# Kernel tuning notes

Hardware: AMD Instinct MI355X
Metric: run time of the kernel (lower is better)

Reference implementation:

```python
import jax, jax.numpy as jnp
import numpy as np

N_NODES = 100000
N_EDGES = 1600000
F_IN, F_HID, F_OUT = 48, 16, 16
K = 2  # kernel_size, dim=1, degree=1 open B-spline -> basis (1-u, u)


def glorot(key, shape):
    fan_in, fan_out = shape[-2], shape[-1]
    s = jnp.sqrt(6.0 / (fan_in + fan_out))
    return jax.random.uniform(key, shape, jnp.float32, -s, s)


def setup_inputs() -> dict:
    key = jax.random.key(0)
    ks = jax.random.split(key, 10)
    x = jax.random.normal(ks[0], (N_NODES, F_IN), jnp.float32)
    edge_attr = jax.random.uniform(ks[1], (N_EDGES, 1), jnp.float32)
    edge_index = jax.random.randint(ks[2], (2, N_EDGES), 0, N_NODES, jnp.int64)
    W1 = glorot(ks[3], (K, F_IN, F_HID))
    root1 = glorot(ks[4], (F_IN, F_HID))
    b1 = jnp.zeros((F_HID,), jnp.float32)
    W2 = glorot(ks[5], (K, F_HID, F_OUT))
    root2 = glorot(ks[6], (F_HID, F_OUT))
    b2 = jnp.zeros((F_OUT,), jnp.float32)
    return {"x": x, "edge_attr": edge_attr, "edge_index": edge_index,
            "W1": W1, "root1": root1, "b1": b1, "W2": W2, "root2": root2, "b2": b2}


def spline_conv(x, edge_index, u, W, root, bias, num_nodes):
    # x: [N,Fin], u: [E] pseudo coords in [0,1], W: [2,Fin,Fout]
    src, dst = edge_index[0], edge_index[1]
    xj = x[src]                                        # [E,Fin] gather
    m = jnp.einsum('ef,kfo->eko', xj, W)               # [E,2,Fout]
    basis = jnp.stack([1.0 - u, u], axis=1)            # linear open B-spline, K=2
    msg = jnp.einsum('ek,eko->eo', basis, m)           # [E,Fout]
    agg = jax.ops.segment_sum(msg, dst, num_segments=num_nodes)
    cnt = jax.ops.segment_sum(jnp.ones_like(msg[:, 0]), dst, num_segments=num_nodes)
    agg = agg / jnp.maximum(cnt, 1.0)[:, None]         # aggr='mean'
    return agg + x @ root + bias                       # root_weight + bias


def reference(x, edge_attr, edge_index, W1, root1, b1, W2, root2, b2):
    u = edge_attr[:, 0]
    h = jax.nn.elu(spline_conv(x, edge_index, u, W1, root1, b1, N_NODES))
    out = spline_conv(h, edge_index, u, W2, root2, b2, N_NODES)
    return jax.nn.log_softmax(out, axis=1)
```

## Files before the change

kernel.cpp:

```cpp
#include <hip/hip_runtime.h>
#include <math.h>

#define N_NODES 100000
#define N_EDGES 1600000
#define NBUK 782
#define BNODES 128
#define CAPSH 12
#define CAP 4096
#define NCHUNK 512
#define CPE 3125
#define NTBLK 1563
#define WS 52
#define RPW (BNODES + 1)

#define SM_LCUR   0
#define SM_GBASE  3128
#define SM_SC     6256
#define SM_UPK    10352
#define SM_SPK    22852
#define SM_UBUK   35352
#define SM_SBUK   41602
#define SM_UDL    47852
#define SM_SDL    50977
#define SM_TOTAL  54144

#define NTL(p) __builtin_nontemporal_load(p)

__device__ __forceinline__ unsigned bf16_rne(float x) {
    unsigned u = __float_as_uint(x);
    return (u + 0x7FFFu + ((u >> 16) & 1u)) >> 16;
}

__device__ __forceinline__ void accq(float acc[4], uint4 w, float uu) {
    acc[0] += fmaf(uu, __uint_as_float(w.x & 0xFFFF0000u), __uint_as_float(w.x << 16));
    acc[1] += fmaf(uu, __uint_as_float(w.y & 0xFFFF0000u), __uint_as_float(w.y << 16));
    acc[2] += fmaf(uu, __uint_as_float(w.z & 0xFFFF0000u), __uint_as_float(w.z << 16));
    acc[3] += fmaf(uu, __uint_as_float(w.w & 0xFFFF0000u), __uint_as_float(w.w << 16));
}

__global__ __launch_bounds__(1024)
void fused_transform_scatter(const float* __restrict__ X,
                             const float* __restrict__ W,
                             const float* __restrict__ root,
                             const float* __restrict__ bias,
                             unsigned* __restrict__ YPH, float* __restrict__ R,
                             const int* __restrict__ src,
                             const int* __restrict__ dst,
                             const float* __restrict__ u,
                             int* __restrict__ cursor,
                             unsigned* __restrict__ pkb,
                             unsigned char* __restrict__ dlb) {
    extern __shared__ char smem[];
    int t = threadIdx.x;
    if (blockIdx.x < NCHUNK) {
        int c = blockIdx.x;
        int* lcur            = (int*)(smem + SM_LCUR);
        int* gbase           = (int*)(smem + SM_GBASE);
        int* sc              = (int*)(smem + SM_SC);
        unsigned* upk        = (unsigned*)(smem + SM_UPK);
        unsigned* spk        = (unsigned*)(smem + SM_SPK);
        unsigned short* ubuk = (unsigned short*)(smem + SM_UBUK);
        unsigned short* sbuk = (unsigned short*)(smem + SM_SBUK);
        unsigned char* udl   = (unsigned char*)(smem + SM_UDL);
        unsigned char* sdl   = (unsigned char*)(smem + SM_SDL);

        for (int i = t; i < NBUK; i += 1024) lcur[i] = 0;
        __syncthreads();
        for (int j = t; j < CPE; j += 1024) {
            int e = c * CPE + j;
            int d = NTL(dst + e);
            float uu = NTL(u + e);
            uu = uu < 0.0f ? 0.0f : (uu > 1.0f ? 1.0f : uu);
            int u15 = (int)fmaf(uu, 32767.0f, 0.5f);
            upk[j] = (unsigned)NTL(src + e) | ((unsigned)u15 << 17);
            udl[j] = (unsigned char)(d & 127);
            int b = d >> 7;
            ubuk[j] = (unsigned short)b;
            atomicAdd(&lcur[b], 1);
        }
        __syncthreads();

        int v = (t < NBUK) ? lcur[t] : 0;
        sc[t] = v;
        __syncthreads();
        for (int off = 1; off < 1024; off <<= 1) {
            int x = (t >= off) ? sc[t - off] : 0;
            __syncthreads();
            sc[t] += x;
            __syncthreads();
        }
        if (t < NBUK) {
            int ex = sc[t] - v;
            lcur[t] = ex;
            int base = (t << CAPSH) + atomicAdd(&cursor[t], v);
            gbase[t] = base - ex;
        }
        __syncthreads();

        for (int j = t; j < CPE; j += 1024) {
            int b = ubuk[j];
            int p = atomicAdd(&lcur[b], 1);
            spk[p] = upk[j];
            sdl[p] = udl[j];
            sbuk[p] = (unsigned short)b;
        }
        __syncthreads();

        for (int j = t; j < CPE; j += 1024) {
            int b = sbuk[j];
            int g = gbase[b] + j;
            if (g < ((b + 1) << CAPSH)) {
                pkb[g] = spk[j];
                dlb[g] = sdl[j];
            }
        }
    } else {
        float* sW0 = (float*)smem;
        float* sWd = (float*)(smem + 3328);
        float* sR  = (float*)(smem + 6656);
        float* sB  = (float*)(smem + 9984);
        int bid = blockIdx.x - NCHUNK;
        for (int i = t; i < 48 * 16; i += 1024) {
            int f = i >> 4, o = i & 15;
            float w0 = W[i];
            float w1 = W[48 * 16 + i];
            sW0[o * WS + f] = w0;
            sWd[o * WS + f] = w1 - w0;
            sR[o * WS + f]  = root[i];
        }
        if (t < 16) sB[t] = bias[t];
        __syncthreads();

        int idx = bid * 1024 + t;
        int n = idx >> 4;
        int o = idx & 15;
        if (n >= N_NODES) return;

        const float4* xr  = (const float4*)(X + (long)n * 48);
        const float4* w0p = (const float4*)(sW0 + o * WS);
        const float4* wdp = (const float4*)(sWd + o * WS);
        const float4* wrp = (const float4*)(sR  + o * WS);
        float a0 = 0.0f, a1 = 0.0f, ar = 0.0f;
#pragma unroll
        for (int fc = 0; fc < 12; ++fc) {
            float4 xv = xr[fc];
            float4 w0 = w0p[fc];
            float4 wd = wdp[fc];
            float4 wr = wrp[fc];
            a0 = fmaf(xv.x, w0.x, a0); a0 = fmaf(xv.y, w0.y, a0);
            a0 = fmaf(xv.z, w0.z, a0); a0 = fmaf(xv.w, w0.w, a0);
            a1 = fmaf(xv.x, wd.x, a1); a1 = fmaf(xv.y, wd.y, a1);
            a1 = fmaf(xv.z, wd.z, a1); a1 = fmaf(xv.w, wd.w, a1);
            ar = fmaf(xv.x, wr.x, ar); ar = fmaf(xv.y, wr.y, ar);
            ar = fmaf(xv.z, wr.z, ar); ar = fmaf(xv.w, wr.w, ar);
        }
        YPH[idx] = bf16_rne(a0) | (bf16_rne(a1) << 16);
        R[idx]   = ar + sB[o];
    }
}

__global__ __launch_bounds__(512)
void aggregate1(const int* __restrict__ cursor,
                unsigned* __restrict__ pkb,
                const unsigned char* __restrict__ dlb,
                int* __restrict__ rptab,
                const uint4* __restrict__ YPH1,
                const float* __restrict__ R1,
                const float* __restrict__ W2,
                const float* __restrict__ root2,
                const float* __restrict__ b2,
                unsigned* __restrict__ YPH2,
                float* __restrict__ R2) {
    __shared__ unsigned spk[CAP];
    __shared__ int rp[RPW];
    __shared__ int cur[BNODES];
    __shared__ float sW0[256], sWd[256], sR[256], sB[16];
    int t = threadIdx.x, b = blockIdx.x;

    if (t < 256) {
        float w0 = W2[t], w1 = W2[256 + t];
        sW0[t] = w0;
        sWd[t] = w1 - w0;
        sR[t]  = root2[t];
    }
    if (t < 16) sB[t] = b2[t];
    if (t < BNODES) cur[t] = 0;
    __syncthreads();

    int cnt = cursor[b];
    if (cnt > CAP) cnt = CAP;
    unsigned* pk = pkb + ((size_t)b << CAPSH);
    const unsigned char* dl = dlb + ((size_t)b << CAPSH);
    int n4 = cnt >> 2, tail = cnt & 3, base4 = cnt & ~3;

    for (int j4 = t; j4 < n4; j4 += 512) {
        unsigned w = NTL((const unsigned*)dl + j4);
        atomicAdd(&cur[w & 255], 1);
        atomicAdd(&cur[(w >> 8) & 255], 1);
        atomicAdd(&cur[(w >> 16) & 255], 1);
        atomicAdd(&cur[w >> 24], 1);
    }
    if (t < tail) atomicAdd(&cur[NTL(dl + base4 + t)], 1);
    __syncthreads();

    int v = 0;
    if (t < BNODES) { v = cur[t]; rp[t] = v; }
    __syncthreads();
    for (int off = 1; off < BNODES; off <<= 1) {
        int x = 0;
        if (t < BNODES && t >= off) x = rp[t - off];
        __syncthreads();
        if (t < BNODES) rp[t] += x;
        __syncthreads();
    }
    if (t < BNODES) { int ex = rp[t] - v; rp[t] = ex; cur[t] = ex; }
    if (t == 0) rp[BNODES] = cnt;
    __syncthreads();

    for (int j4 = t; j4 < n4; j4 += 512) {
        uint4 p = ((const uint4*)pk)[j4];
        unsigned w = NTL((const unsigned*)dl + j4);
        spk[atomicAdd(&cur[w & 255], 1)]         = p.x;
        spk[atomicAdd(&cur[(w >> 8) & 255], 1)]  = p.y;
        spk[atomicAdd(&cur[(w >> 16) & 255], 1)] = p.z;
        spk[atomicAdd(&cur[w >> 24], 1)]         = p.w;
    }
    if (t < tail) {
        int j = base4 + t;
        spk[atomicAdd(&cur[NTL(dl + j)], 1)] = pk[j];
    }
    __syncthreads();

    for (int j = t; j < cnt; j += 512) pk[j] = spk[j];
    if (t < RPW) rptab[b * RPW + t] = rp[t];

    int node = t >> 2, q = t & 3;
    int n = (b << 7) + node;
    int beg = rp[node], end = rp[node + 1];
    int deg = end - beg;
    const float C = 1.0f / 32767.0f;

    float acc[4] = {0.0f, 0.0f, 0.0f, 0.0f};
    int j = beg;
    for (; j + 3 < end; j += 4) {
        unsigned p0 = spk[j], p1 = spk[j + 1], p2 = spk[j + 2], p3 = spk[j + 3];
        uint4 w0 = YPH1[(size_t)(p0 & 0x1FFFFu) * 4 + q];
        uint4 w1 = YPH1[(size_t)(p1 & 0x1FFFFu) * 4 + q];
        uint4 w2 = YPH1[(size_t)(p2 & 0x1FFFFu) * 4 + q];
        uint4 w3 = YPH1[(size_t)(p3 & 0x1FFFFu) * 4 + q];
        accq(acc, w0, (float)(p0 >> 17) * C);
        accq(acc, w1, (float)(p1 >> 17) * C);
        accq(acc, w2, (float)(p2 >> 17) * C);
        accq(acc, w3, (float)(p3 >> 17) * C);
    }
    for (; j < end; ++j) {
        unsigned p = spk[j];
        uint4 w = YPH1[(size_t)(p & 0x1FFFFu) * 4 + q];
        accq(acc, w, (float)(p >> 17) * C);
    }

    if (n < N_NODES) {
        float inv = 1.0f / (deg > 0 ? (float)deg : 1.0f);
        float4 rr = ((const float4*)(R1 + (size_t)n * 16))[q];
        float hq[4], w;
        w = fmaf(acc[0], inv, rr.x); hq[0] = w > 0.0f ? w : expm1f(w);
        w = fmaf(acc[1], inv, rr.y); hq[1] = w > 0.0f ? w : expm1f(w);
        w = fmaf(acc[2], inv, rr.z); hq[2] = w > 0.0f ? w : expm1f(w);
        w = fmaf(acc[3], inv, rr.w); hq[3] = w > 0.0f ? w : expm1f(w);

        int qbase = (t & 63) & ~3;
        float h16[16];
#pragma unroll
        for (int p = 0; p < 4; ++p) {
            h16[4 * p + 0] = __shfl(hq[0], qbase + p);
            h16[4 * p + 1] = __shfl(hq[1], qbase + p);
            h16[4 * p + 2] = __shfl(hq[2], qbase + p);
            h16[4 * p + 3] = __shfl(hq[3], qbase + p);
        }

        float a0[4] = {0, 0, 0, 0}, a1[4] = {0, 0, 0, 0}, ar[4] = {0, 0, 0, 0};
        int o0 = q * 4;
#pragma unroll
        for (int f = 0; f < 16; ++f) {
            float hv = h16[f];
#pragma unroll
            for (int o = 0; o < 4; ++o) {
                a0[o] = fmaf(hv, sW0[f * 16 + o0 + o], a0[o]);
                a1[o] = fmaf(hv, sWd[f * 16 + o0 + o], a1[o]);
                ar[o] = fmaf(hv, sR [f * 16 + o0 + o], ar[o]);
            }
        }
        uint4 yw;
        yw.x = bf16_rne(a0[0]) | (bf16_rne(a1[0]) << 16);
        yw.y = bf16_rne(a0[1]) | (bf16_rne(a1[1]) << 16);
        yw.z = bf16_rne(a0[2]) | (bf16_rne(a1[2]) << 16);
        yw.w = bf16_rne(a0[3]) | (bf16_rne(a1[3]) << 16);
        ((uint4*)YPH2)[(size_t)n * 4 + q] = yw;
        float4 rv;
        rv.x = ar[0] + sB[o0 + 0];
        rv.y = ar[1] + sB[o0 + 1];
        rv.z = ar[2] + sB[o0 + 2];
        rv.w = ar[3] + sB[o0 + 3];
        ((float4*)R2)[(size_t)n * 4 + q] = rv;
    }
}

__global__ __launch_bounds__(512)
void aggregate2(const int* __restrict__ rptab,
                const unsigned* __restrict__ pkb,
                const uint4* __restrict__ YPH2,
                const float* __restrict__ R2,
                float* __restrict__ out) {
    __shared__ int rp[RPW];
    int t = threadIdx.x, b = blockIdx.x;

    if (t < RPW) rp[t] = rptab[b * RPW + t];
    __syncthreads();

    const unsigned* pk = pkb + ((size_t)b << CAPSH);
    int node = t >> 2, q = t & 3;
    int n = (b << 7) + node;
    int beg = rp[node], end = rp[node + 1];
    int deg = end - beg;
    const float C = 1.0f / 32767.0f;

    float acc[4] = {0.0f, 0.0f, 0.0f, 0.0f};
    int j = beg;
    for (; j + 3 < end; j += 4) {
        unsigned p0 = pk[j], p1 = pk[j + 1], p2 = pk[j + 2], p3 = pk[j + 3];
        uint4 w0 = YPH2[(size_t)(p0 & 0x1FFFFu) * 4 + q];
        uint4 w1 = YPH2[(size_t)(p1 & 0x1FFFFu) * 4 + q];
        uint4 w2 = YPH2[(size_t)(p2 & 0x1FFFFu) * 4 + q];
        uint4 w3 = YPH2[(size_t)(p3 & 0x1FFFFu) * 4 + q];
        accq(acc, w0, (float)(p0 >> 17) * C);
        accq(acc, w1, (float)(p1 >> 17) * C);
        accq(acc, w2, (float)(p2 >> 17) * C);
        accq(acc, w3, (float)(p3 >> 17) * C);
    }
    for (; j < end; ++j) {
        unsigned p = pk[j];
        uint4 w = YPH2[(size_t)(p & 0x1FFFFu) * 4 + q];
        accq(acc, w, (float)(p >> 17) * C);
    }

    if (n < N_NODES) {
        float inv = 1.0f / (deg > 0 ? (float)deg : 1.0f);
        float4 rr = ((const float4*)R2)[(size_t)n * 4 + q];
        float v0 = fmaf(acc[0], inv, rr.x);
        float v1 = fmaf(acc[1], inv, rr.y);
        float v2 = fmaf(acc[2], inv, rr.z);
        float v3 = fmaf(acc[3], inv, rr.w);
        float m = fmaxf(fmaxf(v0, v1), fmaxf(v2, v3));
        m = fmaxf(m, __shfl_xor(m, 1));
        m = fmaxf(m, __shfl_xor(m, 2));
        float s = expf(v0 - m) + expf(v1 - m) + expf(v2 - m) + expf(v3 - m);
        s += __shfl_xor(s, 1);
        s += __shfl_xor(s, 2);
        float lse = m + logf(s);
        float4 ov = make_float4(v0 - lse, v1 - lse, v2 - lse, v3 - lse);
        ((float4*)out)[(size_t)n * 4 + q] = ov;
    }
}

extern "C" void kernel_launch(void* const* d_in, const int* in_sizes, int n_in,
                              void* d_out, int out_size, void* d_ws, size_t ws_size,
                              hipStream_t stream) {
    const float* x         = (const float*)d_in[0];
    const float* edge_attr = (const float*)d_in[1];
    const int*   edge_idx  = (const int*)d_in[2];
    const float* W1        = (const float*)d_in[3];
    const float* root1     = (const float*)d_in[4];
    const float* b1        = (const float*)d_in[5];
    const float* W2        = (const float*)d_in[6];
    const float* root2     = (const float*)d_in[7];
    const float* b2        = (const float*)d_in[8];
    float* out = (float*)d_out;

    const int* src = edge_idx;
    const int* dst = edge_idx + N_EDGES;

    char* ws = (char*)d_ws;
    unsigned*      pkb    = (unsigned*)(ws);
    unsigned char* dlb    = (unsigned char*)(ws + 12812288);
    unsigned*      YPH1   = (unsigned*)(ws + 16015360);
    float*         R1     = (float*)(ws + 22415360);
    unsigned*      YPH2   = (unsigned*)(ws + 28815360);
    float*         R2     = (float*)(ws + 35215360);
    int*           cursor = (int*)(ws + 41615360);
    int*           rptab  = (int*)(ws + 41618496);

    hipMemsetAsync(cursor, 0, NBUK * sizeof(int), stream);

    fused_transform_scatter<<<dim3(NCHUNK + NTBLK), 1024, SM_TOTAL, stream>>>(
        x, W1, root1, b1, YPH1, R1, src, dst, edge_attr, cursor, pkb, dlb);

    aggregate1<<<dim3(NBUK), 512, 0, stream>>>(
        cursor, pkb, dlb, rptab, (const uint4*)YPH1, R1, W2, root2, b2, YPH2, R2);

    aggregate2<<<dim3(NBUK), 512, 0, stream>>>(
        rptab, pkb, (const uint4*)YPH2, R2, out);
}
```

Baseline: 179.7 us.

## Replace LDS-staged edge bucketing with global atomics and split node aggregation across lane pairs

```diff
diff --git a/kernel.cpp b/kernel.cpp
--- a/kernel.cpp
+++ b/kernel.cpp
@@ -7,24 +7,16 @@
 #define BNODES 128
 #define CAPSH 12
 #define CAP 4096
-#define NCHUNK 512
-#define CPE 3125
+#define NSBLK 391
 #define NTBLK 1563
 #define WS 52
 #define RPW (BNODES + 1)
-
-#define SM_LCUR   0
-#define SM_GBASE  3128
-#define SM_SC     6256
-#define SM_UPK    10352
-#define SM_SPK    22852
-#define SM_UBUK   35352
-#define SM_SBUK   41602
-#define SM_UDL    47852
-#define SM_SDL    50977
-#define SM_TOTAL  54144
+#define SM_TRANSFORM 10048
 
 #define NTL(p) __builtin_nontemporal_load(p)
+
+typedef int   i32x4 __attribute__((ext_vector_type(4)));
+typedef float f32x4 __attribute__((ext_vector_type(4)));
 
 __device__ __forceinline__ unsigned bf16_rne(float x) {
     unsigned u = __float_as_uint(x);
@@ -52,66 +44,27 @@
                              unsigned char* __restrict__ dlb) {
     extern __shared__ char smem[];
     int t = threadIdx.x;
-    if (blockIdx.x < NCHUNK) {
-        int c = blockIdx.x;
-        int* lcur            = (int*)(smem + SM_LCUR);
-        int* gbase           = (int*)(smem + SM_GBASE);
-        int* sc              = (int*)(smem + SM_SC);
-        unsigned* upk        = (unsigned*)(smem + SM_UPK);
-        unsigned* spk        = (unsigned*)(smem + SM_SPK);
-        unsigned short* ubuk = (unsigned short*)(smem + SM_UBUK);
-        unsigned short* sbuk = (unsigned short*)(smem + SM_SBUK);
-        unsigned char* udl   = (unsigned char*)(smem + SM_UDL);
-        unsigned char* sdl   = (unsigned char*)(smem + SM_SDL);
-
-        for (int i = t; i < NBUK; i += 1024) lcur[i] = 0;
-        __syncthreads();
-        for (int j = t; j < CPE; j += 1024) {
-            int e = c * CPE + j;
-            int d = NTL(dst + e);
-            float uu = NTL(u + e);
-            uu = uu < 0.0f ? 0.0f : (uu > 1.0f ? 1.0f : uu);
-            int u15 = (int)fmaf(uu, 32767.0f, 0.5f);
-            upk[j] = (unsigned)NTL(src + e) | ((unsigned)u15 << 17);
-            udl[j] = (unsigned char)(d & 127);
-            int b = d >> 7;
-            ubuk[j] = (unsigned short)b;
-            atomicAdd(&lcur[b], 1);
-        }
-        __syncthreads();
-
-        int v = (t < NBUK) ? lcur[t] : 0;
-        sc[t] = v;
-        __syncthreads();
-        for (int off = 1; off < 1024; off <<= 1) {
-            int x = (t >= off) ? sc[t - off] : 0;
-            __syncthreads();
-            sc[t] += x;
-            __syncthreads();
-        }
-        if (t < NBUK) {
-            int ex = sc[t] - v;
-            lcur[t] = ex;
-            int base = (t << CAPSH) + atomicAdd(&cursor[t], v);
-            gbase[t] = base - ex;
-        }
-        __syncthreads();
-
-        for (int j = t; j < CPE; j += 1024) {
-            int b = ubuk[j];
-            int p = atomicAdd(&lcur[b], 1);
-            spk[p] = upk[j];
-            sdl[p] = udl[j];
-            sbuk[p] = (unsigned short)b;
-        }
-        __syncthreads();
-
-        for (int j = t; j < CPE; j += 1024) {
-            int b = sbuk[j];
-            int g = gbase[b] + j;
-            if (g < ((b + 1) << CAPSH)) {
-                pkb[g] = spk[j];
-                dlb[g] = sdl[j];
+    if (blockIdx.x < NSBLK) {
+        int gid = blockIdx.x * 1024 + t;
+        int e = gid * 4;
+        if (e < N_EDGES) {
+            i32x4 s4 = NTL((const i32x4*)src + gid);
+            i32x4 d4 = NTL((const i32x4*)dst + gid);
+            f32x4 u4 = NTL((const f32x4*)u + gid);
+#pragma unroll
+            for (int k = 0; k < 4; ++k) {
+                int d = d4[k];
+                float uu = u4[k];
+                uu = uu < 0.0f ? 0.0f : (uu > 1.0f ? 1.0f : uu);
+                int u15 = (int)fmaf(uu, 32767.0f, 0.5f);
+                unsigned pk = (unsigned)s4[k] | ((unsigned)u15 << 17);
+                int b = d >> 7;
+                int off = atomicAdd(&cursor[b], 1);
+                if (off < CAP) {
+                    int g = (b << CAPSH) + off;
+                    pkb[g] = pk;
+                    dlb[g] = (unsigned char)(d & 127);
+                }
             }
         }
     } else {
@@ -119,7 +72,7 @@
         float* sWd = (float*)(smem + 3328);
         float* sR  = (float*)(smem + 6656);
         float* sB  = (float*)(smem + 9984);
-        int bid = blockIdx.x - NCHUNK;
+        int bid = blockIdx.x - NSBLK;
         for (int i = t; i < 48 * 16; i += 1024) {
             int f = i >> 4, o = i & 15;
             float w0 = W[i];
@@ -159,7 +112,7 @@
     }
 }
 
-__global__ __launch_bounds__(512)
+__global__ __launch_bounds__(1024)
 void aggregate1(const int* __restrict__ cursor,
                 unsigned* __restrict__ pkb,
                 const unsigned char* __restrict__ dlb,
@@ -193,7 +146,7 @@
     const unsigned char* dl = dlb + ((size_t)b << CAPSH);
     int n4 = cnt >> 2, tail = cnt & 3, base4 = cnt & ~3;
 
-    for (int j4 = t; j4 < n4; j4 += 512) {
+    for (int j4 = t; j4 < n4; j4 += 1024) {
         unsigned w = NTL((const unsigned*)dl + j4);
         atomicAdd(&cur[w & 255], 1);
         atomicAdd(&cur[(w >> 8) & 255], 1);
@@ -217,7 +170,7 @@
     if (t == 0) rp[BNODES] = cnt;
     __syncthreads();
 
-    for (int j4 = t; j4 < n4; j4 += 512) {
+    for (int j4 = t; j4 < n4; j4 += 1024) {
         uint4 p = ((const uint4*)pk)[j4];
         unsigned w = NTL((const unsigned*)dl + j4);
         spk[atomicAdd(&cur[w & 255], 1)]         = p.x;
@@ -231,19 +184,19 @@
     }
     __syncthreads();
 
-    for (int j = t; j < cnt; j += 512) pk[j] = spk[j];
+    for (int j = t; j < cnt; j += 1024) pk[j] = spk[j];
     if (t < RPW) rptab[b * RPW + t] = rp[t];
 
-    int node = t >> 2, q = t & 3;
+    int node = t >> 3, lane3 = t & 7, q = lane3 & 3, h = lane3 >> 2;
     int n = (b << 7) + node;
     int beg = rp[node], end = rp[node + 1];
     int deg = end - beg;
     const float C = 1.0f / 32767.0f;
 
     float acc[4] = {0.0f, 0.0f, 0.0f, 0.0f};
-    int j = beg;
-    for (; j + 3 < end; j += 4) {
-        unsigned p0 = spk[j], p1 = spk[j + 1], p2 = spk[j + 2], p3 = spk[j + 3];
+    int j = beg + h;
+    for (; j + 6 < end; j += 8) {
+        unsigned p0 = spk[j], p1 = spk[j + 2], p2 = spk[j + 4], p3 = spk[j + 6];
         uint4 w0 = YPH1[(size_t)(p0 & 0x1FFFFu) * 4 + q];
         uint4 w1 = YPH1[(size_t)(p1 & 0x1FFFFu) * 4 + q];
         uint4 w2 = YPH1[(size_t)(p2 & 0x1FFFFu) * 4 + q];
@@ -253,11 +206,13 @@
         accq(acc, w2, (float)(p2 >> 17) * C);
         accq(acc, w3, (float)(p3 >> 17) * C);
     }
-    for (; j < end; ++j) {
+    for (; j < end; j += 2) {
         unsigned p = spk[j];
         uint4 w = YPH1[(size_t)(p & 0x1FFFFu) * 4 + q];
         accq(acc, w, (float)(p >> 17) * C);
     }
+#pragma unroll
+    for (int i = 0; i < 4; ++i) acc[i] += __shfl_xor(acc[i], 4);
 
     if (n < N_NODES) {
         float inv = 1.0f / (deg > 0 ? (float)deg : 1.0f);
@@ -268,14 +223,14 @@
         w = fmaf(acc[2], inv, rr.z); hq[2] = w > 0.0f ? w : expm1f(w);
         w = fmaf(acc[3], inv, rr.w); hq[3] = w > 0.0f ? w : expm1f(w);
 
-        int qbase = (t & 63) & ~3;
+        int b8 = (t & 63) & ~7;
         float h16[16];
 #pragma unroll
         for (int p = 0; p < 4; ++p) {
-            h16[4 * p + 0] = __shfl(hq[0], qbase + p);
-            h16[4 * p + 1] = __shfl(hq[1], qbase + p);
-            h16[4 * p + 2] = __shfl(hq[2], qbase + p);
-            h16[4 * p + 3] = __shfl(hq[3], qbase + p);
+            h16[4 * p + 0] = __shfl(hq[0], b8 + p);
+            h16[4 * p + 1] = __shfl(hq[1], b8 + p);
+            h16[4 * p + 2] = __shfl(hq[2], b8 + p);
+            h16[4 * p + 3] = __shfl(hq[3], b8 + p);
         }
 
         float a0[4] = {0, 0, 0, 0}, a1[4] = {0, 0, 0, 0}, ar[4] = {0, 0, 0, 0};
@@ -290,22 +245,24 @@
                 ar[o] = fmaf(hv, sR [f * 16 + o0 + o], ar[o]);
             }
         }
-        uint4 yw;
-        yw.x = bf16_rne(a0[0]) | (bf16_rne(a1[0]) << 16);
-        yw.y = bf16_rne(a0[1]) | (bf16_rne(a1[1]) << 16);
-        yw.z = bf16_rne(a0[2]) | (bf16_rne(a1[2]) << 16);
-        yw.w = bf16_rne(a0[3]) | (bf16_rne(a1[3]) << 16);
-        ((uint4*)YPH2)[(size_t)n * 4 + q] = yw;
-        float4 rv;
-        rv.x = ar[0] + sB[o0 + 0];
-        rv.y = ar[1] + sB[o0 + 1];
-        rv.z = ar[2] + sB[o0 + 2];
-        rv.w = ar[3] + sB[o0 + 3];
-        ((float4*)R2)[(size_t)n * 4 + q] = rv;
-    }
-}
-
-__global__ __launch_bounds__(512)
+        if (h == 0) {
+            uint4 yw;
+            yw.x = bf16_rne(a0[0]) | (bf16_rne(a1[0]) << 16);
+            yw.y = bf16_rne(a0[1]) | (bf16_rne(a1[1]) << 16);
+            yw.z = bf16_rne(a0[2]) | (bf16_rne(a1[2]) << 16);
+            yw.w = bf16_rne(a0[3]) | (bf16_rne(a1[3]) << 16);
+            ((uint4*)YPH2)[(size_t)n * 4 + q] = yw;
+            float4 rv;
+            rv.x = ar[0] + sB[o0 + 0];
+            rv.y = ar[1] + sB[o0 + 1];
+            rv.z = ar[2] + sB[o0 + 2];
+            rv.w = ar[3] + sB[o0 + 3];
+            ((float4*)R2)[(size_t)n * 4 + q] = rv;
+        }
+    }
+}
+
+__global__ __launch_bounds__(1024)
 void aggregate2(const int* __restrict__ rptab,
                 const unsigned* __restrict__ pkb,
                 const uint4* __restrict__ YPH2,
@@ -318,16 +275,17 @@
     __syncthreads();
 
     const unsigned* pk = pkb + ((size_t)b << CAPSH);
-    int node = t >> 2, q = t & 3;
+    int node = t >> 3, lane3 = t & 7, q = lane3 & 3, h = lane3 >> 2;
     int n = (b << 7) + node;
     int beg = rp[node], end = rp[node + 1];
     int deg = end - beg;
     const float C = 1.0f / 32767.0f;
 
     float acc[4] = {0.0f, 0.0f, 0.0f, 0.0f};
-    int j = beg;
-    for (; j + 3 < end; j += 4) {
-        unsigned p0 = pk[j], p1 = pk[j + 1], p2 = pk[j + 2], p3 = pk[j + 3];
+    int j = beg + h;
+    for (; j + 6 < end; j += 8) {
+        unsigned p0 = NTL(pk + j), p1 = NTL(pk + j + 2);
+        unsigned p2 = NTL(pk + j + 4), p3 = NTL(pk + j + 6);
         uint4 w0 = YPH2[(size_t)(p0 & 0x1FFFFu) * 4 + q];
         uint4 w1 = YPH2[(size_t)(p1 & 0x1FFFFu) * 4 + q];
         uint4 w2 = YPH2[(size_t)(p2 & 0x1FFFFu) * 4 + q];
@@ -337,11 +295,13 @@
         accq(acc, w2, (float)(p2 >> 17) * C);
         accq(acc, w3, (float)(p3 >> 17) * C);
     }
-    for (; j < end; ++j) {
-        unsigned p = pk[j];
+    for (; j < end; j += 2) {
+        unsigned p = NTL(pk + j);
         uint4 w = YPH2[(size_t)(p & 0x1FFFFu) * 4 + q];
         accq(acc, w, (float)(p >> 17) * C);
     }
+#pragma unroll
+    for (int i = 0; i < 4; ++i) acc[i] += __shfl_xor(acc[i], 4);
 
     if (n < N_NODES) {
         float inv = 1.0f / (deg > 0 ? (float)deg : 1.0f);
@@ -357,8 +317,10 @@
         s += __shfl_xor(s, 1);
         s += __shfl_xor(s, 2);
         float lse = m + logf(s);
-        float4 ov = make_float4(v0 - lse, v1 - lse, v2 - lse, v3 - lse);
-        ((float4*)out)[(size_t)n * 4 + q] = ov;
+        if (h == 0) {
+            float4 ov = make_float4(v0 - lse, v1 - lse, v2 - lse, v3 - lse);
+            ((float4*)out)[(size_t)n * 4 + q] = ov;
+        }
     }
 }
 
@@ -391,12 +353,12 @@
 
     hipMemsetAsync(cursor, 0, NBUK * sizeof(int), stream);
 
-    fused_transform_scatter<<<dim3(NCHUNK + NTBLK), 1024, SM_TOTAL, stream>>>(
+    fused_transform_scatter<<<dim3(NSBLK + NTBLK), 1024, SM_TRANSFORM, stream>>>(
         x, W1, root1, b1, YPH1, R1, src, dst, edge_attr, cursor, pkb, dlb);
 
-    aggregate1<<<dim3(NBUK), 512, 0, stream>>>(
+    aggregate1<<<dim3(NBUK), 1024, 0, stream>>>(
         cursor, pkb, dlb, rptab, (const uint4*)YPH1, R1, W2, root2, b2, YPH2, R2);
 
-    aggregate2<<<dim3(NBUK), 512, 0, stream>>>(
+    aggregate2<<<dim3(NBUK), 1024, 0, stream>>>(
         rptab, pkb, (const uint4*)YPH2, R2, out);
 }
```

Result: slower. 530.2 us (+195.0%).

## Pack edge payload and full dst into single 64-bit record with smaller bucket capacity

Applied to the files above, without the earlier changes.

```diff
diff --git a/kernel.cpp b/kernel.cpp
--- a/kernel.cpp
+++ b/kernel.cpp
@@ -5,24 +5,20 @@
 #define N_EDGES 1600000
 #define NBUK 782
 #define BNODES 128
-#define CAPSH 12
-#define CAP 4096
+#define CAP 2560
+#define CAPB (CAP * 8)
 #define NCHUNK 512
 #define CPE 3125
 #define NTBLK 1563
 #define WS 52
 #define RPW (BNODES + 1)
 
-#define SM_LCUR   0
-#define SM_GBASE  3128
-#define SM_SC     6256
-#define SM_UPK    10352
-#define SM_SPK    22852
-#define SM_UBUK   35352
-#define SM_SBUK   41602
-#define SM_UDL    47852
-#define SM_SDL    50977
-#define SM_TOTAL  54144
+#define SM_LCUR  0
+#define SM_GBASE 3128
+#define SM_SC    6256
+#define SM_UPDL  10352
+#define SM_SPDL  35352
+#define SM_TOTAL 60352
 
 #define NTL(p) __builtin_nontemporal_load(p)
 
@@ -48,21 +44,16 @@
                              const int* __restrict__ dst,
                              const float* __restrict__ u,
                              int* __restrict__ cursor,
-                             unsigned* __restrict__ pkb,
-                             unsigned char* __restrict__ dlb) {
+                             unsigned long long* __restrict__ pkd) {
     extern __shared__ char smem[];
     int t = threadIdx.x;
     if (blockIdx.x < NCHUNK) {
         int c = blockIdx.x;
-        int* lcur            = (int*)(smem + SM_LCUR);
-        int* gbase           = (int*)(smem + SM_GBASE);
-        int* sc              = (int*)(smem + SM_SC);
-        unsigned* upk        = (unsigned*)(smem + SM_UPK);
-        unsigned* spk        = (unsigned*)(smem + SM_SPK);
-        unsigned short* ubuk = (unsigned short*)(smem + SM_UBUK);
-        unsigned short* sbuk = (unsigned short*)(smem + SM_SBUK);
-        unsigned char* udl   = (unsigned char*)(smem + SM_UDL);
-        unsigned char* sdl   = (unsigned char*)(smem + SM_SDL);
+        int* lcur = (int*)(smem + SM_LCUR);
+        int* gbase = (int*)(smem + SM_GBASE);
+        int* sc = (int*)(smem + SM_SC);
+        unsigned long long* updl = (unsigned long long*)(smem + SM_UPDL);
+        unsigned long long* spdl = (unsigned long long*)(smem + SM_SPDL);
 
         for (int i = t; i < NBUK; i += 1024) lcur[i] = 0;
         __syncthreads();
@@ -72,11 +63,10 @@
             float uu = NTL(u + e);
             uu = uu < 0.0f ? 0.0f : (uu > 1.0f ? 1.0f : uu);
             int u15 = (int)fmaf(uu, 32767.0f, 0.5f);
-            upk[j] = (unsigned)NTL(src + e) | ((unsigned)u15 << 17);
-            udl[j] = (unsigned char)(d & 127);
-            int b = d >> 7;
-            ubuk[j] = (unsigned short)b;
-            atomicAdd(&lcur[b], 1);
+            unsigned pk32 = (unsigned)NTL(src + e) | ((unsigned)u15 << 17);
+            updl[j] = (unsigned long long)pk32 |
+                      ((unsigned long long)(unsigned)d << 32);
+            atomicAdd(&lcur[d >> 7], 1);
         }
         __syncthreads();
 
@@ -92,27 +82,25 @@
         if (t < NBUK) {
             int ex = sc[t] - v;
             lcur[t] = ex;
-            int base = (t << CAPSH) + atomicAdd(&cursor[t], v);
+            int base = t * CAP + atomicAdd(&cursor[t], v);
             gbase[t] = base - ex;
         }
         __syncthreads();
 
         for (int j = t; j < CPE; j += 1024) {
-            int b = ubuk[j];
+            unsigned long long w = updl[j];
+            int b = (int)(w >> 39) & 0x3FF;
             int p = atomicAdd(&lcur[b], 1);
-            spk[p] = upk[j];
-            sdl[p] = udl[j];
-            sbuk[p] = (unsigned short)b;
+            spdl[p] = w;
         }
         __syncthreads();
 
         for (int j = t; j < CPE; j += 1024) {
-            int b = sbuk[j];
+            unsigned long long w = spdl[j];
+            int b = (int)(w >> 39) & 0x3FF;
             int g = gbase[b] + j;
-            if (g < ((b + 1) << CAPSH)) {
-                pkb[g] = spk[j];
-                dlb[g] = sdl[j];
-            }
+            if (g < (b + 1) * CAP)
+                pkd[g] = w;
         }
     } else {
         float* sW0 = (float*)smem;
@@ -161,8 +149,7 @@
 
 __global__ __launch_bounds__(512)
 void aggregate1(const int* __restrict__ cursor,
-                unsigned* __restrict__ pkb,
-                const unsigned char* __restrict__ dlb,
+                unsigned long long* __restrict__ pkd,
                 int* __restrict__ rptab,
                 const uint4* __restrict__ YPH1,
                 const float* __restrict__ R1,
@@ -171,6 +158,7 @@
                 const float* __restrict__ b2,
                 unsigned* __restrict__ YPH2,
                 float* __restrict__ R2) {
+    __shared__ unsigned long long updl[CAP];
     __shared__ unsigned spk[CAP];
     __shared__ int rp[RPW];
     __shared__ int cur[BNODES];
@@ -189,18 +177,14 @@
 
     int cnt = cursor[b];
     if (cnt > CAP) cnt = CAP;
-    unsigned* pk = pkb + ((size_t)b << CAPSH);
-    const unsigned char* dl = dlb + ((size_t)b << CAPSH);
-    int n4 = cnt >> 2, tail = cnt & 3, base4 = cnt & ~3;
-
-    for (int j4 = t; j4 < n4; j4 += 512) {
-        unsigned w = NTL((const unsigned*)dl + j4);
-        atomicAdd(&cur[w & 255], 1);
-        atomicAdd(&cur[(w >> 8) & 255], 1);
-        atomicAdd(&cur[(w >> 16) & 255], 1);
-        atomicAdd(&cur[w >> 24], 1);
-    }
-    if (t < tail) atomicAdd(&cur[NTL(dl + base4 + t)], 1);
+    unsigned long long* gp =
+        (unsigned long long*)((char*)pkd + (size_t)b * CAPB);
+
+    for (int j = t; j < cnt; j += 512) {
+        unsigned long long w = NTL(gp + j);
+        updl[j] = w;
+        atomicAdd(&cur[(int)(w >> 32) & 127], 1);
+    }
     __syncthreads();
 
     int v = 0;
@@ -217,21 +201,15 @@
     if (t == 0) rp[BNODES] = cnt;
     __syncthreads();
 
-    for (int j4 = t; j4 < n4; j4 += 512) {
-        uint4 p = ((const uint4*)pk)[j4];
-        unsigned w = NTL((const unsigned*)dl + j4);
-        spk[atomicAdd(&cur[w & 255], 1)]         = p.x;
-        spk[atomicAdd(&cur[(w >> 8) & 255], 1)]  = p.y;
-        spk[atomicAdd(&cur[(w >> 16) & 255], 1)] = p.z;
-        spk[atomicAdd(&cur[w >> 24], 1)]         = p.w;
-    }
-    if (t < tail) {
-        int j = base4 + t;
-        spk[atomicAdd(&cur[NTL(dl + j)], 1)] = pk[j];
-    }
-    __syncthreads();
-
-    for (int j = t; j < cnt; j += 512) pk[j] = spk[j];
+    for (int j = t; j < cnt; j += 512) {
+        unsigned long long w = updl[j];
+        int pos = atomicAdd(&cur[(int)(w >> 32) & 127], 1);
+        spk[pos] = (unsigned)w;
+    }
+    __syncthreads();
+
+    unsigned* gs = (unsigned*)((char*)pkd + (size_t)b * CAPB);
+    for (int j = t; j < cnt; j += 512) gs[j] = spk[j];
     if (t < RPW) rptab[b * RPW + t] = rp[t];
 
     int node = t >> 2, q = t & 3;
@@ -307,7 +285,7 @@
 
 __global__ __launch_bounds__(512)
 void aggregate2(const int* __restrict__ rptab,
-                const unsigned* __restrict__ pkb,
+                const unsigned long long* __restrict__ pkd,
                 const uint4* __restrict__ YPH2,
                 const float* __restrict__ R2,
                 float* __restrict__ out) {
@@ -317,7 +295,7 @@
     if (t < RPW) rp[t] = rptab[b * RPW + t];
     __syncthreads();
 
-    const unsigned* pk = pkb + ((size_t)b << CAPSH);
+    const unsigned* pk = (const unsigned*)((const char*)pkd + (size_t)b * CAPB);
     int node = t >> 2, q = t & 3;
     int n = (b << 7) + node;
     int beg = rp[node], end = rp[node + 1];
@@ -327,7 +305,8 @@
     float acc[4] = {0.0f, 0.0f, 0.0f, 0.0f};
     int j = beg;
     for (; j + 3 < end; j += 4) {
-        unsigned p0 = pk[j], p1 = pk[j + 1], p2 = pk[j + 2], p3 = pk[j + 3];
+        unsigned p0 = NTL(pk + j), p1 = NTL(pk + j + 1);
+        unsigned p2 = NTL(pk + j + 2), p3 = NTL(pk + j + 3);
         uint4 w0 = YPH2[(size_t)(p0 & 0x1FFFFu) * 4 + q];
         uint4 w1 = YPH2[(size_t)(p1 & 0x1FFFFu) * 4 + q];
         uint4 w2 = YPH2[(size_t)(p2 & 0x1FFFFu) * 4 + q];
@@ -338,7 +317,7 @@
         accq(acc, w3, (float)(p3 >> 17) * C);
     }
     for (; j < end; ++j) {
-        unsigned p = pk[j];
+        unsigned p = NTL(pk + j);
         uint4 w = YPH2[(size_t)(p & 0x1FFFFu) * 4 + q];
         accq(acc, w, (float)(p >> 17) * C);
     }
@@ -380,23 +359,22 @@
     const int* dst = edge_idx + N_EDGES;
 
     char* ws = (char*)d_ws;
-    unsigned*      pkb    = (unsigned*)(ws);
-    unsigned char* dlb    = (unsigned char*)(ws + 12812288);
-    unsigned*      YPH1   = (unsigned*)(ws + 16015360);
-    float*         R1     = (float*)(ws + 22415360);
-    unsigned*      YPH2   = (unsigned*)(ws + 28815360);
-    float*         R2     = (float*)(ws + 35215360);
-    int*           cursor = (int*)(ws + 41615360);
-    int*           rptab  = (int*)(ws + 41618496);
+    unsigned long long* pkd = (unsigned long long*)(ws);
+    unsigned* YPH1 = (unsigned*)(ws + 16015360);
+    float*    R1   = (float*)(ws + 22415360);
+    unsigned* YPH2 = (unsigned*)(ws + 28815360);
+    float*    R2   = (float*)(ws + 35215360);
+    int*      cursor = (int*)(ws + 41615360);
+    int*      rptab  = (int*)(ws + 41618496);
 
     hipMemsetAsync(cursor, 0, NBUK * sizeof(int), stream);
 
     fused_transform_scatter<<<dim3(NCHUNK + NTBLK), 1024, SM_TOTAL, stream>>>(
-        x, W1, root1, b1, YPH1, R1, src, dst, edge_attr, cursor, pkb, dlb);
+        x, W1, root1, b1, YPH1, R1, src, dst, edge_attr, cursor, pkd);
 
     aggregate1<<<dim3(NBUK), 512, 0, stream>>>(
-        cursor, pkb, dlb, rptab, (const uint4*)YPH1, R1, W2, root2, b2, YPH2, R2);
+        cursor, pkd, rptab, (const uint4*)YPH1, R1, W2, root2, b2, YPH2, R2);
 
     aggregate2<<<dim3(NBUK), 512, 0, stream>>>(
-        rptab, pkb, (const uint4*)YPH2, R2, out);
-}
+        rptab, pkd, (const uint4*)YPH2, R2, out);
+}
```

Measured after the change: 180.1 us. Within noise of the previous version (+0.2%).
